# Kernel optimization log

Hardware: AMD Instinct MI355X
Metric: run time of the kernel (lower is better)

Reference implementation:

```python
import jax, jax.numpy as jnp
import numpy as np
from jax import lax

DT = 1.0 / 120.0      # system dt from SystemModel(dt=1/120)
G = 9.81              # gravity for friction force
K_SIGN = 100.0        # smooth sign() sharpness (tanh surrogate, differentiable)
TWO_PI = 2.0 * np.pi


def setup_inputs() -> dict:
    key = jax.random.key(0)
    k1, k2, k3, k4 = jax.random.split(key, 4)
    N, T = 8192, 64
    params = jax.random.uniform(k1, (4,), jnp.float32, 0.05, 0.5)           # friction, damping, tableRes, rimFriction
    covariance_params = jax.random.normal(k2, (7,), jnp.float32) * 0.5 - 5.0  # log-variances
    init_state = jax.random.normal(k3, (N, 6), jnp.float32) * 0.5            # [x, y, vx, vy, theta, omega]
    measurements = jax.random.normal(k4, (N, T, 3), jnp.float32) * 0.5       # [x, y, theta] per step
    return {"params": params, "covariance_params": covariance_params,
            "init_state": init_state, "measurements": measurements}


def reference(params, covariance_params, init_state, measurements):
    """Batched EKF over N segments (vectorized over the Python segment loop of the
    original) with lax.scan over the segment_size timesteps. Returns the mean
    log-likelihood loss: mean over segments of sum_t 0.5*(logdet(S_t) + y_t^T S_t^{-1} y_t),
    with the +-2*pi angle-wrap on the theta innovation as in the original."""
    dyna = jnp.abs(params)
    fric, damp = dyna[0], dyna[1]

    cp = covariance_params
    R = jnp.diag(jnp.exp(cp[:3]))                                            # 3x3 measurement noise
    Q = jnp.diag(jnp.exp(jnp.stack([cp[3], cp[3], cp[4], cp[4], cp[5], cp[6]])))  # 6x6 process noise

    N = init_state.shape[0]
    P0 = jnp.broadcast_to(jnp.eye(6, dtype=init_state.dtype) * 0.01, (N, 6, 6))
    midx = jnp.array([0, 1, 4])
    H = jnp.zeros((3, 6), init_state.dtype).at[0, 0].set(1.).at[1, 1].set(1.).at[2, 4].set(1.)
    I6 = jnp.eye(6, dtype=init_state.dtype)

    def predict(x):
        # free-slide puck dynamics: damping + dry friction (smooth sign)
        pos, vel, th, om = x[:, 0:2], x[:, 2:4], x[:, 4], x[:, 5]
        t = jnp.tanh(K_SIGN * vel)
        pos_n = pos + DT * vel
        vel_n = vel - DT * (damp * vel + fric * G * t)
        th_n = th + DT * om
        om_n = om - DT * damp * om
        return jnp.concatenate([pos_n, vel_n, th_n[:, None], om_n[:, None]], axis=1), t

    def jacobian_F(t):
        # analytic Jacobian of predict; [N,6,6]
        N_ = t.shape[0]
        dv = 1.0 - DT * (damp + fric * G * K_SIGN * (1.0 - t * t))           # [N,2]
        F = jnp.broadcast_to(I6, (N_, 6, 6))
        F = F.at[:, 0, 2].set(DT).at[:, 1, 3].set(DT).at[:, 4, 5].set(DT)
        F = F.at[:, 2, 2].set(dv[:, 0]).at[:, 3, 3].set(dv[:, 1])
        F = F.at[:, 5, 5].set(1.0 - DT * damp)
        return F

    def step(carry, z):
        x, P = carry
        x_pred, t = predict(x)
        F = jacobian_F(t)
        P_pred = jnp.einsum('nij,njk,nlk->nil', F, P, F) + Q                  # F P F^T + Q

        y = z - x_pred[:, midx]                                               # innovation [N,3]
        ang = y[:, 2]
        ang = jnp.where(ang > 1.5 * np.pi, ang - TWO_PI,
                        jnp.where(ang < -1.5 * np.pi, ang + TWO_PI, ang))
        y = y.at[:, 2].set(ang)

        S = P_pred[:, midx, :][:, :, midx] + R                                # [N,3,3]
        Sinv = jnp.linalg.inv(S)
        K = jnp.einsum('nij,njk->nik', P_pred[:, :, midx], Sinv)              # [N,6,3]

        x_new = x_pred + jnp.einsum('nij,nj->ni', K, y)
        KH = jnp.einsum('nij,jk->nik', K, H)                                  # [N,6,6]
        P_new = jnp.einsum('nij,njk->nik', I6 - KH, P_pred)

        _, logdet = jnp.linalg.slogdet(S)
        maha = jnp.einsum('ni,nij,nj->n', y, Sinv, y)
        loss_t = 0.5 * jnp.sum(logdet + maha)
        return (x_new, P_new), loss_t

    (_, _), losses = lax.scan(step, (init_state, P0),
                              jnp.transpose(measurements, (1, 0, 2)))        # scan over T
    return jnp.sum(losses) / N
```

## Files before the change

kernel.cpp:

```cpp
#include <hip/hip_runtime.h>
#include <math.h>

#define DT_STEP (1.0f / 120.0f)
#define G_ACC 9.81f
#define KS 100.0f

typedef float v2f __attribute__((ext_vector_type(2)));

__device__ __forceinline__ float frcp(float x) { return __builtin_amdgcn_rcpf(x); }
__device__ __forceinline__ v2f fma2(v2f a, v2f b, v2f c) { return __builtin_elementwise_fma(a, b, c); }

__device__ __forceinline__ void ekf_step_pk(
    const float damp, const float fG, const float fGKS,
    const v2f R, const float Qp, const float Qv,
    v2f& s0, v2f& s1, v2f& a, v2f& b, v2f& c,
    const v2f z, v2f& maha, v2f& sprod)
{
    v2f e;
    e.x = __expf(2.0f * KS * s1.x);
    e.y = __expf(2.0f * KS * s1.y);
    v2f u;
    u.x = 2.0f * frcp(e.x + 1.0f);
    u.y = 2.0f * frcp(e.y + 1.0f);
    const v2f th = 1.0f - u;

    const v2f s0p = fma2((v2f)DT_STEP, s1, s0);
    const v2f s1p = s1 - DT_STEP * fma2((v2f)damp, s1, fG * th);
    const v2f dv = 1.0f - DT_STEP * fma2((v2f)fGKS, u * (2.0f - u), (v2f)damp);

    const v2f M00 = fma2((v2f)DT_STEP, b, a);
    const v2f M01 = fma2((v2f)DT_STEP, c, b);
    const v2f Pp00 = fma2((v2f)DT_STEP, M01, M00) + Qp;
    const v2f Pp01 = dv * M01;
    const v2f Pp11 = fma2(dv * dv, c, (v2f)Qv);

    const v2f y = z - s0p;

    const v2f S = Pp00 + R;
    v2f Si;
    Si.x = frcp(S.x);
    Si.y = frcp(S.y);
    const v2f K0 = Pp00 * Si;
    const v2f K1 = Pp01 * Si;

    s0 = fma2(K0, y, s0p);
    s1 = fma2(K1, y, s1p);

    a = R * K0;
    b = R * K1;
    c = fma2(-K1, Pp01, Pp11);

    maha = fma2(y * y, Si, maha);
    sprod *= S;
}

__device__ __forceinline__ void ekf_step_th(
    const float a55, const float R, const float Qp, const float Qv,
    float& s0, float& s1, float& a, float& b, float& c,
    const float z, float& maha, float& sprod)
{
    const float PI15 = 4.7123889803846899f;
    const float TWOPI = 6.2831853071795865f;

    const float s0p = fmaf(DT_STEP, s1, s0);
    const float s1p = a55 * s1;
    const float dv = a55;

    const float M00 = fmaf(DT_STEP, b, a);
    const float M01 = fmaf(DT_STEP, c, b);
    const float Pp00 = fmaf(DT_STEP, M01, M00) + Qp;
    const float Pp01 = dv * M01;
    const float Pp11 = fmaf(dv * dv, c, Qv);

    float y = z - s0p;
    if (y > PI15) y -= TWOPI;
    else if (y < -PI15) y += TWOPI;

    const float S = Pp00 + R;
    const float Si = frcp(S);
    const float K0 = Pp00 * Si;
    const float K1 = Pp01 * Si;

    s0 = fmaf(K0, y, s0p);
    s1 = fmaf(K1, y, s1p);

    a = R * K0;
    b = R * K1;
    c = fmaf(-K1, Pp01, Pp11);

    maha = fmaf(y * y, Si, maha);
    sprod *= S;
}

template <int TT>
__global__ __launch_bounds__(64, 1) void ekf_pk_kernel(
    const float* __restrict__ params, const float* __restrict__ cp,
    const float* __restrict__ init_state, const float* __restrict__ meas,
    float* __restrict__ out, int N)
{
    const int lane = threadIdx.x & 63;
    const int seg = blockIdx.x * 64 + lane;
    float local = 0.0f;

    const float fric = fabsf(params[0]);
    const float damp = fabsf(params[1]);
    const float* zrow = meas + (size_t)seg * (3 * TT);
    const float* sb = init_state + (size_t)seg * 6;

    if (blockIdx.y == 0) {
        v2f z2[TT];
#pragma unroll
        for (int t = 0; t < TT; t++) {
            z2[t].x = zrow[3 * t + 0];
            z2[t].y = zrow[3 * t + 1];
        }

        const float fG = fric * G_ACC;
        const float fGKS = fG * KS;
        v2f R;
        R.x = __expf(cp[0]);
        R.y = __expf(cp[1]);
        const float Qp = __expf(cp[3]);
        const float Qv = __expf(cp[4]);

        v2f s0, s1;
        s0.x = sb[0]; s0.y = sb[1];
        s1.x = sb[2]; s1.y = sb[3];
        v2f a = 0.01f, b = (v2f)0.0f, c = 0.01f;
        v2f maha = (v2f)0.0f;
        float logsum = 0.0f;

        static_assert(TT % 8 == 0, "TT multiple of 8");
#pragma unroll
        for (int g = 0; g < TT / 8; g++) {
            v2f sprod = 1.0f;
#pragma unroll
            for (int k = 0; k < 8; k++)
                ekf_step_pk(damp, fG, fGKS, R, Qp, Qv, s0, s1, a, b, c, z2[g * 8 + k], maha, sprod);
            logsum += __logf(sprod.x) + __logf(sprod.y);
        }
        local = logsum + maha.x + maha.y;
    } else {
        float z[TT];
#pragma unroll
        for (int t = 0; t < TT; t++) z[t] = zrow[3 * t + 2];

        const float a55 = 1.0f - DT_STEP * damp;
        const float R = __expf(cp[2]);
        const float Qp = __expf(cp[5]);
        const float Qv = __expf(cp[6]);

        float s0 = sb[4], s1 = sb[5];
        float a = 0.01f, b = 0.0f, c = 0.01f;
        float maha = 0.0f, logsum = 0.0f;
#pragma unroll
        for (int g = 0; g < TT / 8; g++) {
            float sprod = 1.0f;
#pragma unroll
            for (int k = 0; k < 8; k++)
                ekf_step_th(a55, R, Qp, Qv, s0, s1, a, b, c, z[g * 8 + k], maha, sprod);
            logsum += __logf(sprod);
        }
        local = logsum + maha;
    }

#pragma unroll
    for (int off = 32; off > 0; off >>= 1)
        local += __shfl_down(local, off, 64);

    if (lane == 0) atomicAdd(out, local * 0.5f / (float)N);
}

__global__ __launch_bounds__(64, 1) void ekf_gen_kernel(
    const float* __restrict__ params, const float* __restrict__ cp,
    const float* __restrict__ init_state, const float* __restrict__ meas,
    float* __restrict__ out, int N, int T)
{
    const int lane = threadIdx.x & 63;
    const int seg = blockIdx.x * 64 + lane;
    const int ft = blockIdx.y;
    float local = 0.0f;

    if (seg < N) {
        const float fric = fabsf(params[0]);
        const float damp = fabsf(params[1]);
        const float fG = fric * G_ACC;
        const float fGKS = fG * KS;
        const float a55 = 1.0f - DT_STEP * damp;
        const float R  = __expf(cp[ft]);
        const float Qp = __expf((ft == 2) ? cp[5] : cp[3]);
        const float Qv = __expf((ft == 2) ? cp[6] : cp[4]);
        const float* sb = init_state + (size_t)seg * 6;
        float s0 = sb[(ft == 2) ? 4 : ft];
        float s1 = sb[(ft == 2) ? 5 : ft + 2];
        float a = 0.01f, b = 0.0f, c = 0.01f;
        float maha = 0.0f, logsum = 0.0f;

        const float* zrow = meas + (size_t)seg * (3 * T) + ft;
        for (int t = 0; t < T; t++) {
            const float z = zrow[3 * t];
            if (ft == 2) {
                float sprod = 1.0f;
                ekf_step_th(a55, R, Qp, Qv, s0, s1, a, b, c, z, maha, sprod);
                logsum += __logf(sprod);
            } else {
                v2f s0v = (v2f)s0, s1v = (v2f)s1, av = (v2f)a, bv = (v2f)b, cv = (v2f)c;
                v2f mv = (v2f)0.0f, sp = (v2f)1.0f;
                ekf_step_pk(damp, fG, fGKS, (v2f)R, Qp, Qv, s0v, s1v, av, bv, cv, (v2f)z, mv, sp);
                s0 = s0v.x; s1 = s1v.x; a = av.x; b = bv.x; c = cv.x;
                maha += mv.x; logsum += __logf(sp.x);
            }
        }
        local = logsum + maha;
    }

#pragma unroll
    for (int off = 32; off > 0; off >>= 1)
        local += __shfl_down(local, off, 64);
    if (lane == 0) atomicAdd(out, local * 0.5f / (float)N);
}

extern "C" void kernel_launch(void* const* d_in, const int* in_sizes, int n_in,
                              void* d_out, int out_size, void* d_ws, size_t ws_size,
                              hipStream_t stream) {
    const float* params     = (const float*)d_in[0];
    const float* cov_params = (const float*)d_in[1];
    const float* init_state = (const float*)d_in[2];
    const float* meas       = (const float*)d_in[3];
    float* out = (float*)d_out;

    const int N = in_sizes[2] / 6;
    const int T = in_sizes[3] / (N * 3);

    if (T == 64 && (N % 64) == 0) {
        dim3 grid(N / 64, 2);
        ekf_pk_kernel<64><<<grid, 64, 0, stream>>>(params, cov_params, init_state, meas, out, N);
    } else {
        hipMemsetAsync(out, 0, sizeof(float), stream);
        dim3 grid((N + 63) / 64, 3);
        ekf_gen_kernel<<<grid, 64, 0, stream>>>(params, cov_params, init_state, meas, out, N, T);
    }
}
```

Before: 72.40 us.

## Split x/y filters into separate blocks and simplify position step algebra

New measurement: 74.52 us. +2.9%, slower.

```diff
diff --git a/kernel.cpp b/kernel.cpp
--- a/kernel.cpp
+++ b/kernel.cpp
@@ -5,52 +5,45 @@
 #define G_ACC 9.81f
 #define KS 100.0f
 
-typedef float v2f __attribute__((ext_vector_type(2)));
-
 __device__ __forceinline__ float frcp(float x) { return __builtin_amdgcn_rcpf(x); }
-__device__ __forceinline__ v2f fma2(v2f a, v2f b, v2f c) { return __builtin_elementwise_fma(a, b, c); }
-
-__device__ __forceinline__ void ekf_step_pk(
-    const float damp, const float fG, const float fGKS,
-    const v2f R, const float Qp, const float Qv,
-    v2f& s0, v2f& s1, v2f& a, v2f& b, v2f& c,
-    const v2f z, v2f& maha, v2f& sprod)
-{
-    v2f e;
-    e.x = __expf(2.0f * KS * s1.x);
-    e.y = __expf(2.0f * KS * s1.y);
-    v2f u;
-    u.x = 2.0f * frcp(e.x + 1.0f);
-    u.y = 2.0f * frcp(e.y + 1.0f);
-    const v2f th = 1.0f - u;
-
-    const v2f s0p = fma2((v2f)DT_STEP, s1, s0);
-    const v2f s1p = s1 - DT_STEP * fma2((v2f)damp, s1, fG * th);
-    const v2f dv = 1.0f - DT_STEP * fma2((v2f)fGKS, u * (2.0f - u), (v2f)damp);
-
-    const v2f M00 = fma2((v2f)DT_STEP, b, a);
-    const v2f M01 = fma2((v2f)DT_STEP, c, b);
-    const v2f Pp00 = fma2((v2f)DT_STEP, M01, M00) + Qp;
-    const v2f Pp01 = dv * M01;
-    const v2f Pp11 = fma2(dv * dv, c, (v2f)Qv);
-
-    const v2f y = z - s0p;
-
-    const v2f S = Pp00 + R;
-    v2f Si;
-    Si.x = frcp(S.x);
-    Si.y = frcp(S.y);
-    const v2f K0 = Pp00 * Si;
-    const v2f K1 = Pp01 * Si;
-
-    s0 = fma2(K0, y, s0p);
-    s1 = fma2(K1, y, s1p);
+
+__device__ __forceinline__ void ekf_step_pos(
+    const float C, const float negD, const float twoD, const float fourB,
+    const float R, const float QpR, const float Qv,
+    float& s0, float& s1, float& a, float& b, float& c,
+    const float z, float& maha, float& sprod)
+{
+    float e = __expf(200.0f * s1);
+    e = fminf(e, 1e30f);
+    const float ep1 = e + 1.0f;
+
+    const float M01 = fmaf(DT_STEP, c, b);
+    const float T0  = fmaf(DT_STEP, b, a);
+    const float S   = fmaf(DT_STEP, M01, T0) + QpR;
+
+    const float rc = frcp(ep1 * S);
+    const float Si = rc * ep1;
+    const float r  = rc * S;
+
+    const float dv  = fmaf(r, fmaf(fourB, r, -fourB), C);
+    const float s0p = fmaf(DT_STEP, s1, s0);
+    const float s1p = fmaf(twoD, r, fmaf(C, s1, negD));
+
+    const float P01 = dv * M01;
+    const float P11 = fmaf(dv * dv, c, Qv);
+
+    const float y  = z - s0p;
+    const float K0 = fmaf(-R, Si, 1.0f);
+    const float K1 = P01 * Si;
+
+    s0 = fmaf(K0, y, s0p);
+    s1 = fmaf(K1, y, s1p);
 
     a = R * K0;
     b = R * K1;
-    c = fma2(-K1, Pp01, Pp11);
-
-    maha = fma2(y * y, Si, maha);
+    c = fmaf(-K1, P01, P11);
+
+    maha = fmaf(y * y, Si, maha);
     sprod *= S;
 }
 
@@ -93,66 +86,34 @@
 }
 
 template <int TT>
-__global__ __launch_bounds__(64, 1) void ekf_pk_kernel(
+__global__ __launch_bounds__(64, 1) void ekf3_kernel(
     const float* __restrict__ params, const float* __restrict__ cp,
     const float* __restrict__ init_state, const float* __restrict__ meas,
     float* __restrict__ out, int N)
 {
     const int lane = threadIdx.x & 63;
     const int seg = blockIdx.x * 64 + lane;
-    float local = 0.0f;
-
-    const float fric = fabsf(params[0]);
+    const int ft = blockIdx.y;
+
     const float damp = fabsf(params[1]);
-    const float* zrow = meas + (size_t)seg * (3 * TT);
     const float* sb = init_state + (size_t)seg * 6;
-
-    if (blockIdx.y == 0) {
-        v2f z2[TT];
-#pragma unroll
-        for (int t = 0; t < TT; t++) {
-            z2[t].x = zrow[3 * t + 0];
-            z2[t].y = zrow[3 * t + 1];
-        }
-
-        const float fG = fric * G_ACC;
-        const float fGKS = fG * KS;
-        v2f R;
-        R.x = __expf(cp[0]);
-        R.y = __expf(cp[1]);
-        const float Qp = __expf(cp[3]);
-        const float Qv = __expf(cp[4]);
-
-        v2f s0, s1;
-        s0.x = sb[0]; s0.y = sb[1];
-        s1.x = sb[2]; s1.y = sb[3];
-        v2f a = 0.01f, b = (v2f)0.0f, c = 0.01f;
-        v2f maha = (v2f)0.0f;
-        float logsum = 0.0f;
-
-        static_assert(TT % 8 == 0, "TT multiple of 8");
-#pragma unroll
-        for (int g = 0; g < TT / 8; g++) {
-            v2f sprod = 1.0f;
-#pragma unroll
-            for (int k = 0; k < 8; k++)
-                ekf_step_pk(damp, fG, fGKS, R, Qp, Qv, s0, s1, a, b, c, z2[g * 8 + k], maha, sprod);
-            logsum += __logf(sprod.x) + __logf(sprod.y);
-        }
-        local = logsum + maha.x + maha.y;
-    } else {
-        float z[TT];
-#pragma unroll
-        for (int t = 0; t < TT; t++) z[t] = zrow[3 * t + 2];
-
+    const float* zp = meas + (size_t)seg * (3 * TT) + ft;
+
+    float z[TT];
+#pragma unroll
+    for (int t = 0; t < TT; t++) z[t] = zp[3 * t];
+
+    float a = 0.01f, b = 0.0f, c = 0.01f;
+    float maha = 0.0f, logsum = 0.0f;
+
+    static_assert(TT % 8 == 0, "TT multiple of 8");
+
+    if (ft == 2) {
         const float a55 = 1.0f - DT_STEP * damp;
-        const float R = __expf(cp[2]);
+        const float R  = __expf(cp[2]);
         const float Qp = __expf(cp[5]);
         const float Qv = __expf(cp[6]);
-
         float s0 = sb[4], s1 = sb[5];
-        float a = 0.01f, b = 0.0f, c = 0.01f;
-        float maha = 0.0f, logsum = 0.0f;
 #pragma unroll
         for (int g = 0; g < TT / 8; g++) {
             float sprod = 1.0f;
@@ -161,8 +122,30 @@
                 ekf_step_th(a55, R, Qp, Qv, s0, s1, a, b, c, z[g * 8 + k], maha, sprod);
             logsum += __logf(sprod);
         }
-        local = logsum + maha;
+    } else {
+        const float fric = fabsf(params[0]);
+        const float fG   = fric * G_ACC;
+        const float C    = 1.0f - DT_STEP * damp;
+        const float D    = DT_STEP * fG;
+        const float negD = -D;
+        const float twoD = 2.0f * D;
+        const float fourB = 4.0f * DT_STEP * fG * KS;
+        const float R  = __expf(cp[ft]);
+        const float Qp = __expf(cp[3]);
+        const float Qv = __expf(cp[4]);
+        const float QpR = Qp + R;
+        float s0 = sb[ft], s1 = sb[ft + 2];
+#pragma unroll
+        for (int g = 0; g < TT / 8; g++) {
+            float sprod = 1.0f;
+#pragma unroll
+            for (int k = 0; k < 8; k++)
+                ekf_step_pos(C, negD, twoD, fourB, R, QpR, Qv, s0, s1, a, b, c, z[g * 8 + k], maha, sprod);
+            logsum += __logf(sprod);
+        }
     }
+
+    float local = logsum + maha;
 
 #pragma unroll
     for (int off = 32; off > 0; off >>= 1)
@@ -184,32 +167,32 @@
     if (seg < N) {
         const float fric = fabsf(params[0]);
         const float damp = fabsf(params[1]);
-        const float fG = fric * G_ACC;
-        const float fGKS = fG * KS;
-        const float a55 = 1.0f - DT_STEP * damp;
+        const float fG   = fric * G_ACC;
+        const float a55  = 1.0f - DT_STEP * damp;
+        const float C    = a55;
+        const float D    = DT_STEP * fG;
+        const float negD = -D;
+        const float twoD = 2.0f * D;
+        const float fourB = 4.0f * DT_STEP * fG * KS;
         const float R  = __expf(cp[ft]);
         const float Qp = __expf((ft == 2) ? cp[5] : cp[3]);
         const float Qv = __expf((ft == 2) ? cp[6] : cp[4]);
+        const float QpR = Qp + R;
         const float* sb = init_state + (size_t)seg * 6;
         float s0 = sb[(ft == 2) ? 4 : ft];
         float s1 = sb[(ft == 2) ? 5 : ft + 2];
         float a = 0.01f, b = 0.0f, c = 0.01f;
         float maha = 0.0f, logsum = 0.0f;
 
-        const float* zrow = meas + (size_t)seg * (3 * T) + ft;
+        const float* zp = meas + (size_t)seg * (3 * T) + ft;
         for (int t = 0; t < T; t++) {
-            const float z = zrow[3 * t];
-            if (ft == 2) {
-                float sprod = 1.0f;
-                ekf_step_th(a55, R, Qp, Qv, s0, s1, a, b, c, z, maha, sprod);
-                logsum += __logf(sprod);
-            } else {
-                v2f s0v = (v2f)s0, s1v = (v2f)s1, av = (v2f)a, bv = (v2f)b, cv = (v2f)c;
-                v2f mv = (v2f)0.0f, sp = (v2f)1.0f;
-                ekf_step_pk(damp, fG, fGKS, (v2f)R, Qp, Qv, s0v, s1v, av, bv, cv, (v2f)z, mv, sp);
-                s0 = s0v.x; s1 = s1v.x; a = av.x; b = bv.x; c = cv.x;
-                maha += mv.x; logsum += __logf(sp.x);
-            }
+            const float zt = zp[3 * t];
+            float sprod = 1.0f;
+            if (ft == 2)
+                ekf_step_th(a55, R, Qp, Qv, s0, s1, a, b, c, zt, maha, sprod);
+            else
+                ekf_step_pos(C, negD, twoD, fourB, R, QpR, Qv, s0, s1, a, b, c, zt, maha, sprod);
+            logsum += __logf(sprod);
         }
         local = logsum + maha;
     }
@@ -233,8 +216,8 @@
     const int T = in_sizes[3] / (N * 3);
 
     if (T == 64 && (N % 64) == 0) {
-        dim3 grid(N / 64, 2);
-        ekf_pk_kernel<64><<<grid, 64, 0, stream>>>(params, cov_params, init_state, meas, out, N);
+        dim3 grid(N / 64, 3);
+        ekf3_kernel<64><<<grid, 64, 0, stream>>>(params, cov_params, init_state, meas, out, N);
     } else {
         hipMemsetAsync(out, 0, sizeof(float), stream);
         dim3 grid((N + 63) / 64, 3);
```
